# Kernel optimization log

Hardware: AMD Instinct MI355X
Metric: run time of the kernel (lower is better)

## Reference

```python
import jax, jax.numpy as jnp
import numpy as np

EMBED_DIM = 131
SCALE = jnp.sqrt(jnp.float32(131.0))


def setup_inputs() -> dict:
    key = jax.random.key(0)
    ks = jax.random.split(key, 9)
    B, N, D = 8, 2048, EMBED_DIM
    s = 1.0 / np.sqrt(D)  # torch Linear default init scale (uniform bound)
    return {
        "query": jax.random.normal(ks[0], (B, N, D), dtype=jnp.float32),
        "key": jax.random.normal(ks[1], (B, N, D), dtype=jnp.float32),
        "value": jax.random.normal(ks[2], (B, N, D), dtype=jnp.float32),
        "Wq": jax.random.uniform(ks[3], (D, D), jnp.float32, -s, s),
        "bq": jax.random.uniform(ks[4], (D,), jnp.float32, -s, s),
        "Wk": jax.random.uniform(ks[5], (D, D), jnp.float32, -s, s),
        "bk": jax.random.uniform(ks[6], (D,), jnp.float32, -s, s),
        "Wv": jax.random.uniform(ks[7], (D, D), jnp.float32, -s, s),
        "bv": jax.random.uniform(ks[8], (D,), jnp.float32, -s, s),
    }


def reference(query, key, value, Wq, bq, Wk, bk, Wv, bv):
    # Linear projections (torch Linear: x @ W.T + b)
    Q = jnp.einsum("bnd,ed->bne", query, Wq) + bq  # [B, N, D]
    K = jnp.einsum("bnd,ed->bne", key, Wk) + bk    # [B, N, D]
    V = jnp.einsum("bnd,ed->bne", value, Wv) + bv  # [B, N, D]
    # Full attention with hardcoded scale sqrt(131)
    scores = jnp.einsum("bqd,bkd->bqk", Q, K) / SCALE  # [B, N, N]
    weights = jax.nn.softmax(scores, axis=-1)
    return jnp.einsum("bqk,bkd->bqd", weights, V)  # [B, N, D]
```

## Files before the change

kernel.cpp:

```cpp
#include <hip/hip_runtime.h>

#define B_ 8
#define N_ 2048
#define D_ 131
#define COSTR 133
#define SXSTR 164
#define CSTR 168
#define TSTR 72

typedef __attribute__((ext_vector_type(8))) short s16x8;
typedef __attribute__((ext_vector_type(16))) float f32x16;

__device__ __forceinline__ ushort f2bf(float x) {
  uint u = __float_as_uint(x);
  u += 0x7fffu + ((u >> 16) & 1u);
  return (ushort)(u >> 16);
}
__device__ __forceinline__ float bf2f(ushort h) {
  return __uint_as_float(((uint)h) << 16);
}
__device__ __forceinline__ uint bfpair(float a, float b) {
  uint ua = __float_as_uint(a);
  ua += 0x7fffu + ((ua >> 16) & 1u);
  uint ub = __float_as_uint(b);
  ub += 0x7fffu + ((ub >> 16) & 1u);
  return (ua >> 16) | (ub & 0xffff0000u);
}

__device__ __forceinline__ size_t rf32_idx(int nt, int ch, int l) {
  return ((size_t)(nt * 9 + ch) * 64 + l) * 8;
}
__device__ __forceinline__ size_t vf32_idx(int kt, int t2, int dt, int l) {
  return ((size_t)(((kt * 2) + t2) * 5 + dt) * 64 + l) * 8;
}
__device__ __forceinline__ size_t wf32_idx(int p, int h, int et, int ch, int l) {
  return ((size_t)((((p * 2 + h) * 5 + et) * 9) + ch) * 64 + l) * 8;
}

__global__ void cast_w_kernel(const float* __restrict__ Wq,
                              const float* __restrict__ Wk,
                              const float* __restrict__ Wv,
                              ushort* __restrict__ Whl) {
  const int p = blockIdx.x;
  const float* __restrict__ W = (p == 0) ? Wq : (p == 1) ? Wk : Wv;
  for (int i = threadIdx.x; i < 5 * 9 * 64; i += blockDim.x) {
    const int et = i / 576;
    const int rem = i - et * 576;
    const int ch = rem >> 6;
    const int l = rem & 63;
    const int e = et * 32 + (l & 31);
    s16x8 hi, lo;
#pragma unroll
    for (int j = 0; j < 8; ++j) {
      const int d = ch * 16 + (l >> 5) * 8 + j;
      const float val = (e < D_ && d < D_) ? W[e * D_ + d] : 0.f;
      const ushort h = f2bf(val);
      hi[j] = (short)h;
      lo[j] = (short)f2bf(val - bf2f(h));
    }
    *(s16x8*)(Whl + wf32_idx(p, 0, et, ch, l)) = hi;
    *(s16x8*)(Whl + wf32_idx(p, 1, et, ch, l)) = lo;
  }
}

template <int ET0, int NET>
__device__ __forceinline__ void compute_acc(const float* sX,
                                            const ushort* __restrict__ Whl,
                                            int p, int tg, int l,
                                            f32x16 acc[3]) {
  const int l31 = l & 31, hi = l >> 5;
#pragma unroll
  for (int ch = 0; ch < 9; ++ch) {
    const float* xp = sX + (size_t)(32 * tg + l31) * SXSTR + ch * 16 + hi * 8;
    const float4 x0 = *(const float4*)xp;
    const float4 x1 = *(const float4*)(xp + 4);
    const float xv[8] = {x0.x, x0.y, x0.z, x0.w, x1.x, x1.y, x1.z, x1.w};
    s16x8 ah, al;
#pragma unroll
    for (int j = 0; j < 8; ++j) {
      const ushort h = f2bf(xv[j]);
      ah[j] = (short)h;
      al[j] = (short)f2bf(xv[j] - bf2f(h));
    }
    s16x8 bh[NET], bl[NET];
#pragma unroll
    for (int u = 0; u < NET; ++u) {
      bh[u] = *(const s16x8*)(Whl + wf32_idx(p, 0, ET0 + u, ch, l));
      bl[u] = *(const s16x8*)(Whl + wf32_idx(p, 1, ET0 + u, ch, l));
    }
#pragma unroll
    for (int u = 0; u < NET; ++u) {
      acc[u] = __builtin_amdgcn_mfma_f32_32x32x16_bf16(ah, bh[u], acc[u], 0, 0, 0);
      acc[u] = __builtin_amdgcn_mfma_f32_32x32x16_bf16(al, bh[u], acc[u], 0, 0, 0);
      acc[u] = __builtin_amdgcn_mfma_f32_32x32x16_bf16(ah, bl[u], acc[u], 0, 0, 0);
    }
  }
}

template <int ET0, int NET>
__device__ __forceinline__ void epiQK(const f32x16 acc[3], ushort* sC,
                                      const float* sB, int tg, int l,
                                      bool scale) {
  const int l31 = l & 31, hi = l >> 5;
  const float ISC = 0.08737040566610379f;
#pragma unroll
  for (int u = 0; u < NET; ++u) {
    const int e = 32 * (ET0 + u) + l31;
    const float bval = sB[e];
#pragma unroll
    for (int r = 0; r < 16; ++r) {
      const int tok = 32 * tg + (r & 3) + 8 * (r >> 2) + 4 * hi;
      float val = acc[u][r] + bval;
      if (scale) val *= ISC;
      sC[(size_t)tok * CSTR + e] = f2bf(val);
    }
  }
}

template <int ET0, int NET>
__device__ __forceinline__ void epiV(const f32x16 acc[3], ushort* sT,
                                     const float* sB, int tg, int l) {
  const int l31 = l & 31, hi = l >> 5;
#pragma unroll
  for (int u = 0; u < NET; ++u) {
    const int e = 32 * (ET0 + u) + l31;
    if (e < D_) {
      const float bval = sB[e];
#pragma unroll
      for (int g = 0; g < 4; ++g) {
        const float v0 = acc[u][4 * g + 0] + bval;
        const float v1 = acc[u][4 * g + 1] + bval;
        const float v2 = acc[u][4 * g + 2] + bval;
        const float v3 = acc[u][4 * g + 3] + bval;
        uint2 pk;
        pk.x = bfpair(v0, v1);
        pk.y = bfpair(v2, v3);
        *(uint2*)(sT + (size_t)e * TSTR + 32 * tg + 8 * g + 4 * hi) = pk;
      }
    }
  }
}

__global__ __launch_bounds__(256, 3) void proj_gemm(
    const float* __restrict__ q, const float* __restrict__ k,
    const float* __restrict__ v, const float* __restrict__ bq,
    const float* __restrict__ bk, const float* __restrict__ bv,
    const ushort* __restrict__ Whl, ushort* __restrict__ Qf,
    ushort* __restrict__ Kf, ushort* __restrict__ Vf) {
  const int p = blockIdx.y;
  const float* __restrict__ x = (p == 0) ? q : (p == 1) ? k : v;
  const float* __restrict__ bias = (p == 0) ? bq : (p == 1) ? bk : bv;

  __shared__ __align__(16) char smem[64 * SXSTR * 4];
  float* sX = (float*)smem;
  ushort* sC = (ushort*)smem;
  ushort* sT = (ushort*)smem;
  __shared__ float sB[160];

  const int tid = threadIdx.x;
  const int r0 = blockIdx.x * 64;

  {
    const float* __restrict__ xbase = x + (size_t)r0 * D_;
    for (int i = tid; i < 64 * D_ / 4; i += 256) {
      const float4 v4 = *(const float4*)(xbase + i * 4);
      const float vv[4] = {v4.x, v4.y, v4.z, v4.w};
#pragma unroll
      for (int j = 0; j < 4; ++j) {
        const int nl = i * 4 + j;
        const int r = nl / D_;
        const int d = nl - r * D_;
        sX[r * SXSTR + d] = vv[j];
      }
    }
    for (int i = tid; i < 64 * 33; i += 256) {
      const int r = i / 33;
      sX[r * SXSTR + D_ + (i - r * 33)] = 0.f;
    }
  }
  if (tid < 160) sB[tid] = (tid < D_) ? bias[tid] : 0.f;
  __syncthreads();

  const int w = tid >> 6;
  const int l = tid & 63;
  const int tg = w & 1;
  const int eh = w >> 1;

  f32x16 acc[3];
  acc[0] = f32x16{};
  acc[1] = f32x16{};
  acc[2] = f32x16{};
  if (eh == 0)
    compute_acc<0, 3>(sX, Whl, p, tg, l, acc);
  else
    compute_acc<3, 2>(sX, Whl, p, tg, l, acc);

  __syncthreads();

  if (p < 2) {
    if (eh == 0)
      epiQK<0, 3>(acc, sC, sB, tg, l, p == 0);
    else
      epiQK<3, 2>(acc, sC, sB, tg, l, p == 0);
    __syncthreads();
    ushort* __restrict__ dst = (p == 0) ? Qf : Kf;
    const int nt0 = r0 >> 5;
    for (int i = tid; i < 2 * 9 * 64; i += 256) {
      const int ntl = i / 576;
      const int rem = i - ntl * 576;
      const int ch = rem >> 6;
      const int l2 = rem & 63;
      const s16x8 fr = *(const s16x8*)(sC + (size_t)(32 * ntl + (l2 & 31)) * CSTR +
                                       ch * 16 + (l2 >> 5) * 8);
      *(s16x8*)(dst + rf32_idx(nt0 + ntl, ch, l2)) = fr;
    }
  } else {
    for (int i = tid; i < 29 * 64; i += 256) {
      const int e = D_ + (i >> 6);
      sT[(size_t)e * TSTR + (i & 63)] = (e == D_) ? (ushort)0x3F80 : (ushort)0;
    }
    if (eh == 0)
      epiV<0, 3>(acc, sT, sB, tg, l);
    else
      epiV<3, 2>(acc, sT, sB, tg, l);
    __syncthreads();
    const int kt0 = r0 >> 5;
    for (int i = tid; i < 2 * 2 * 5 * 64; i += 256) {
      const int ktl = i / 640;
      const int rem = i - ktl * 640;
      const int t2 = rem / 320;
      const int rem2 = rem - t2 * 320;
      const int dt = rem2 >> 6;
      const int l2 = rem2 & 63;
      const s16x8 fr = *(const s16x8*)(sT + (size_t)(32 * dt + (l2 & 31)) * TSTR +
                                       32 * ktl + 16 * t2 + 8 * (l2 >> 5));
      *(s16x8*)(Vf + vf32_idx(kt0 + ktl, t2, dt, l2)) = fr;
    }
  }
}

__global__ __launch_bounds__(256, 2) void attn_mfma(
    const ushort* __restrict__ Qf, const ushort* __restrict__ Kf,
    const ushort* __restrict__ Vf, float* __restrict__ out) {
  const int id = blockIdx.x;
  const int b = id & 7;
  const int qg = id >> 3;
  const int tid = threadIdx.x;
  const int w = tid >> 6;
  const int l = tid & 63;
  const int l31 = l & 31;
  const int hi = l >> 5;

  __shared__ ushort sQ[9 * 64 * 8];
  __shared__ float cO[4][32][COSTR];
  __shared__ float cm[4][32];

  {
    const uint4* src = (const uint4*)(Qf + rf32_idx(b * 64 + qg, 0, 0));
    uint4* dq = (uint4*)sQ;
    for (int i = tid; i < 576; i += 256) dq[i] = src[i];
  }
  s16x8 kA[9], kB[9];
  const int ktbase = b * 64 + w * 16;
#pragma unroll
  for (int ch = 0; ch < 9; ++ch)
    kA[ch] = *(const s16x8*)(Kf + rf32_idx(ktbase, ch, l));
  __syncthreads();

  f32x16 o[5];
#pragma unroll
  for (int dt = 0; dt < 5; ++dt) o[dt] = f32x16{};
  float mreg = -1e30f;

  auto tile_body = [&](s16x8(&KC)[9], s16x8(&KN)[9], int ktg, int ktgn) {
    s16x8 vf[2][5];
#pragma unroll
    for (int t2 = 0; t2 < 2; ++t2)
#pragma unroll
      for (int dt = 0; dt < 5; ++dt)
        vf[t2][dt] = *(const s16x8*)(Vf + vf32_idx(ktg, t2, dt, l));
#pragma unroll
    for (int ch = 0; ch < 9; ++ch)
      KN[ch] = *(const s16x8*)(Kf + rf32_idx(ktgn, ch, l));
    f32x16 s = f32x16{};
#pragma unroll
    for (int ch = 0; ch < 9; ++ch) {
      const s16x8 qc = *(const s16x8*)(sQ + (ch * 64 + l) * 8);
      s = __builtin_amdgcn_mfma_f32_32x32x16_bf16(KC[ch], qc, s, 0, 0, 0);
    }
    float tm = s[0];
#pragma unroll
    for (int r = 1; r < 16; ++r) tm = fmaxf(tm, s[r]);
    tm = fmaxf(tm, __shfl_xor(tm, 32, 64));
    if (__any(tm > mreg)) {
      const float mo = mreg;
      const float mn = fmaxf(mo, tm);
      mreg = mn;
      const float f = __expf(mo - mn);
      float fr[16];
#pragma unroll
      for (int r = 0; r < 16; ++r)
        fr[r] = __shfl(f, (r & 3) + 8 * (r >> 2) + 4 * hi, 64);
#pragma unroll
      for (int dt = 0; dt < 5; ++dt)
#pragma unroll
        for (int r = 0; r < 16; ++r) o[dt][r] *= fr[r];
    }
    float pp[16];
#pragma unroll
    for (int r = 0; r < 16; ++r) pp[r] = __expf(s[r] - mreg);
    uint pk0[4], pk1[4];
#pragma unroll
    for (int wd = 0; wd < 4; ++wd) {
      pk0[wd] = bfpair(pp[2 * wd], pp[2 * wd + 1]);
      pk1[wd] = bfpair(pp[8 + 2 * wd], pp[8 + 2 * wd + 1]);
    }
    s16x8 pa[2];
    {
      const uint x0 = __shfl_xor(hi ? pk0[0] : pk0[2], 32, 64);
      const uint x1 = __shfl_xor(hi ? pk0[1] : pk0[3], 32, 64);
      uint4 u;
      u.x = hi ? x0 : pk0[0];
      u.y = hi ? x1 : pk0[1];
      u.z = hi ? pk0[2] : x0;
      u.w = hi ? pk0[3] : x1;
      pa[0] = *(s16x8*)&u;
    }
    {
      const uint x0 = __shfl_xor(hi ? pk1[0] : pk1[2], 32, 64);
      const uint x1 = __shfl_xor(hi ? pk1[1] : pk1[3], 32, 64);
      uint4 u;
      u.x = hi ? x0 : pk1[0];
      u.y = hi ? x1 : pk1[1];
      u.z = hi ? pk1[2] : x0;
      u.w = hi ? pk1[3] : x1;
      pa[1] = *(s16x8*)&u;
    }
#pragma unroll
    for (int t2 = 0; t2 < 2; ++t2)
#pragma unroll
      for (int dt = 0; dt < 5; ++dt)
        o[dt] = __builtin_amdgcn_mfma_f32_32x32x16_bf16(pa[t2], vf[t2][dt],
                                                        o[dt], 0, 0, 0);
  };

  for (int i = 0; i < 8; ++i) {
    const int kt = ktbase + 2 * i;
    tile_body(kA, kB, kt, kt + 1);
    tile_body(kB, kA, kt + 1, (i < 7) ? kt + 2 : kt + 1);
  }

  if (l < 32) cm[w][l] = mreg;
#pragma unroll
  for (int dt = 0; dt < 5; ++dt) {
    const int d = 32 * dt + l31;
    if (d <= D_) {
#pragma unroll
      for (int r = 0; r < 16; ++r) {
        const int row = (r & 3) + 8 * (r >> 2) + 4 * hi;
        cO[w][row][d] = o[dt][r];
      }
    }
  }
  __syncthreads();
  for (int rr = 0; rr < 8; ++rr) {
    const int row = w * 8 + rr;
    const float m0 = cm[0][row], m1 = cm[1][row];
    const float m2 = cm[2][row], m3 = cm[3][row];
    const float M = fmaxf(fmaxf(m0, m1), fmaxf(m2, m3));
    const float e0 = __expf(m0 - M);
    const float e1 = __expf(m1 - M);
    const float e2 = __expf(m2 - M);
    const float e3 = __expf(m3 - M);
    const float lsum = cO[0][row][D_] * e0 + cO[1][row][D_] * e1 +
                       cO[2][row][D_] * e2 + cO[3][row][D_] * e3;
    const float inv = 1.f / lsum;
    float* orow = out + ((size_t)b * N_ + qg * 32 + row) * D_;
    for (int d = l; d < D_; d += 64) {
      const float val = cO[0][row][d] * e0 + cO[1][row][d] * e1 +
                        cO[2][row][d] * e2 + cO[3][row][d] * e3;
      orow[d] = val * inv;
    }
  }
}

extern "C" void kernel_launch(void* const* d_in, const int* in_sizes, int n_in,
                              void* d_out, int out_size, void* d_ws,
                              size_t ws_size, hipStream_t stream) {
  const float* q = (const float*)d_in[0];
  const float* k = (const float*)d_in[1];
  const float* v = (const float*)d_in[2];
  const float* Wq = (const float*)d_in[3];
  const float* bq = (const float*)d_in[4];
  const float* Wk = (const float*)d_in[5];
  const float* bk = (const float*)d_in[6];
  const float* Wv = (const float*)d_in[7];
  const float* bv = (const float*)d_in[8];
  float* out = (float*)d_out;

  char* wsb = (char*)d_ws;
  ushort* Qf = (ushort*)(wsb);
  ushort* Kf = (ushort*)(wsb + 4718592);
  ushort* Vf = (ushort*)(wsb + 9437184);
  ushort* Whl = (ushort*)(wsb + 14680064);

  hipLaunchKernelGGL(cast_w_kernel, dim3(3), dim3(256), 0, stream, Wq, Wk, Wv,
                     Whl);
  hipLaunchKernelGGL(proj_gemm, dim3(256, 3), dim3(256), 0, stream, q, k, v,
                     bq, bk, bv, Whl, Qf, Kf, Vf);
  hipLaunchKernelGGL(attn_mfma, dim3(512), dim3(256), 0, stream, Qf, Kf, Vf,
                     out);
}
```

Measured before the change: 68.93 us.

## Process two query tiles per block to reuse K/V fragments

Each attention block now handles 64 query rows (two 32-row tiles) instead of 32, sharing each loaded K and V fragment across both tiles. The grid shrinks from 512 to 256 blocks. The launch bound drops to one block per SM because doubled accumulators raise register pressure. This halves global K/V traffic per query row, but lowers occupancy and leaves fewer blocks than there are CUs on MI355X (256), which risks poor load balance and less latency hiding.

```diff
diff --git a/kernel.cpp b/kernel.cpp
--- a/kernel.cpp
+++ b/kernel.cpp
@@ -239,26 +239,26 @@
   }
 }
 
-__global__ __launch_bounds__(256, 2) void attn_mfma(
+__global__ __launch_bounds__(256, 1) void attn_mfma(
     const ushort* __restrict__ Qf, const ushort* __restrict__ Kf,
     const ushort* __restrict__ Vf, float* __restrict__ out) {
   const int id = blockIdx.x;
   const int b = id & 7;
-  const int qg = id >> 3;
+  const int qg2 = id >> 3;
   const int tid = threadIdx.x;
   const int w = tid >> 6;
   const int l = tid & 63;
   const int l31 = l & 31;
   const int hi = l >> 5;
 
-  __shared__ ushort sQ[9 * 64 * 8];
+  __shared__ ushort sQ[2 * 9 * 64 * 8];
   __shared__ float cO[4][32][COSTR];
   __shared__ float cm[4][32];
 
   {
-    const uint4* src = (const uint4*)(Qf + rf32_idx(b * 64 + qg, 0, 0));
+    const uint4* src = (const uint4*)(Qf + rf32_idx(b * 64 + qg2 * 2, 0, 0));
     uint4* dq = (uint4*)sQ;
-    for (int i = tid; i < 576; i += 256) dq[i] = src[i];
+    for (int i = tid; i < 1152; i += 256) dq[i] = src[i];
   }
   s16x8 kA[9], kB[9];
   const int ktbase = b * 64 + w * 16;
@@ -267,10 +267,13 @@
     kA[ch] = *(const s16x8*)(Kf + rf32_idx(ktbase, ch, l));
   __syncthreads();
 
-  f32x16 o[5];
-#pragma unroll
-  for (int dt = 0; dt < 5; ++dt) o[dt] = f32x16{};
-  float mreg = -1e30f;
+  f32x16 o0[5], o1[5];
+#pragma unroll
+  for (int dt = 0; dt < 5; ++dt) {
+    o0[dt] = f32x16{};
+    o1[dt] = f32x16{};
+  }
+  float mreg0 = -1e30f, mreg1 = -1e30f;
 
   auto tile_body = [&](s16x8(&KC)[9], s16x8(&KN)[9], int ktg, int ktgn) {
     s16x8 vf[2][5];
@@ -282,66 +285,72 @@
 #pragma unroll
     for (int ch = 0; ch < 9; ++ch)
       KN[ch] = *(const s16x8*)(Kf + rf32_idx(ktgn, ch, l));
-    f32x16 s = f32x16{};
+    f32x16 s0 = f32x16{}, s1 = f32x16{};
 #pragma unroll
     for (int ch = 0; ch < 9; ++ch) {
-      const s16x8 qc = *(const s16x8*)(sQ + (ch * 64 + l) * 8);
-      s = __builtin_amdgcn_mfma_f32_32x32x16_bf16(KC[ch], qc, s, 0, 0, 0);
-    }
-    float tm = s[0];
-#pragma unroll
-    for (int r = 1; r < 16; ++r) tm = fmaxf(tm, s[r]);
-    tm = fmaxf(tm, __shfl_xor(tm, 32, 64));
-    if (__any(tm > mreg)) {
-      const float mo = mreg;
-      const float mn = fmaxf(mo, tm);
-      mreg = mn;
-      const float f = __expf(mo - mn);
-      float fr[16];
-#pragma unroll
-      for (int r = 0; r < 16; ++r)
-        fr[r] = __shfl(f, (r & 3) + 8 * (r >> 2) + 4 * hi, 64);
-#pragma unroll
-      for (int dt = 0; dt < 5; ++dt)
-#pragma unroll
-        for (int r = 0; r < 16; ++r) o[dt][r] *= fr[r];
-    }
-    float pp[16];
-#pragma unroll
-    for (int r = 0; r < 16; ++r) pp[r] = __expf(s[r] - mreg);
-    uint pk0[4], pk1[4];
-#pragma unroll
-    for (int wd = 0; wd < 4; ++wd) {
-      pk0[wd] = bfpair(pp[2 * wd], pp[2 * wd + 1]);
-      pk1[wd] = bfpair(pp[8 + 2 * wd], pp[8 + 2 * wd + 1]);
-    }
-    s16x8 pa[2];
-    {
-      const uint x0 = __shfl_xor(hi ? pk0[0] : pk0[2], 32, 64);
-      const uint x1 = __shfl_xor(hi ? pk0[1] : pk0[3], 32, 64);
-      uint4 u;
-      u.x = hi ? x0 : pk0[0];
-      u.y = hi ? x1 : pk0[1];
-      u.z = hi ? pk0[2] : x0;
-      u.w = hi ? pk0[3] : x1;
-      pa[0] = *(s16x8*)&u;
-    }
-    {
-      const uint x0 = __shfl_xor(hi ? pk1[0] : pk1[2], 32, 64);
-      const uint x1 = __shfl_xor(hi ? pk1[1] : pk1[3], 32, 64);
-      uint4 u;
-      u.x = hi ? x0 : pk1[0];
-      u.y = hi ? x1 : pk1[1];
-      u.z = hi ? pk1[2] : x0;
-      u.w = hi ? pk1[3] : x1;
-      pa[1] = *(s16x8*)&u;
-    }
-#pragma unroll
-    for (int t2 = 0; t2 < 2; ++t2)
-#pragma unroll
-      for (int dt = 0; dt < 5; ++dt)
-        o[dt] = __builtin_amdgcn_mfma_f32_32x32x16_bf16(pa[t2], vf[t2][dt],
-                                                        o[dt], 0, 0, 0);
+      const s16x8 qc0 = *(const s16x8*)(sQ + (ch * 64 + l) * 8);
+      const s16x8 qc1 = *(const s16x8*)(sQ + ((9 + ch) * 64 + l) * 8);
+      s0 = __builtin_amdgcn_mfma_f32_32x32x16_bf16(KC[ch], qc0, s0, 0, 0, 0);
+      s1 = __builtin_amdgcn_mfma_f32_32x32x16_bf16(KC[ch], qc1, s1, 0, 0, 0);
+    }
+    auto softmax_pv = [&](f32x16& s, float& mreg, f32x16(&og)[5]) {
+      float tm = s[0];
+#pragma unroll
+      for (int r = 1; r < 16; ++r) tm = fmaxf(tm, s[r]);
+      tm = fmaxf(tm, __shfl_xor(tm, 32, 64));
+      if (__any(tm > mreg)) {
+        const float mo = mreg;
+        const float mn = fmaxf(mo, tm);
+        mreg = mn;
+        const float f = __expf(mo - mn);
+        float fr[16];
+#pragma unroll
+        for (int r = 0; r < 16; ++r)
+          fr[r] = __shfl(f, (r & 3) + 8 * (r >> 2) + 4 * hi, 64);
+#pragma unroll
+        for (int dt = 0; dt < 5; ++dt)
+#pragma unroll
+          for (int r = 0; r < 16; ++r) og[dt][r] *= fr[r];
+      }
+      float pp[16];
+#pragma unroll
+      for (int r = 0; r < 16; ++r) pp[r] = __expf(s[r] - mreg);
+      uint pk0[4], pk1[4];
+#pragma unroll
+      for (int wd = 0; wd < 4; ++wd) {
+        pk0[wd] = bfpair(pp[2 * wd], pp[2 * wd + 1]);
+        pk1[wd] = bfpair(pp[8 + 2 * wd], pp[8 + 2 * wd + 1]);
+      }
+      s16x8 pa[2];
+      {
+        const uint x0 = __shfl_xor(hi ? pk0[0] : pk0[2], 32, 64);
+        const uint x1 = __shfl_xor(hi ? pk0[1] : pk0[3], 32, 64);
+        uint4 u;
+        u.x = hi ? x0 : pk0[0];
+        u.y = hi ? x1 : pk0[1];
+        u.z = hi ? pk0[2] : x0;
+        u.w = hi ? pk0[3] : x1;
+        pa[0] = *(s16x8*)&u;
+      }
+      {
+        const uint x0 = __shfl_xor(hi ? pk1[0] : pk1[2], 32, 64);
+        const uint x1 = __shfl_xor(hi ? pk1[1] : pk1[3], 32, 64);
+        uint4 u;
+        u.x = hi ? x0 : pk1[0];
+        u.y = hi ? x1 : pk1[1];
+        u.z = hi ? pk1[2] : x0;
+        u.w = hi ? pk1[3] : x1;
+        pa[1] = *(s16x8*)&u;
+      }
+#pragma unroll
+      for (int t2 = 0; t2 < 2; ++t2)
+#pragma unroll
+        for (int dt = 0; dt < 5; ++dt)
+          og[dt] = __builtin_amdgcn_mfma_f32_32x32x16_bf16(pa[t2], vf[t2][dt],
+                                                           og[dt], 0, 0, 0);
+    };
+    softmax_pv(s0, mreg0, o0);
+    softmax_pv(s1, mreg1, o1);
   };
 
   for (int i = 0; i < 8; ++i) {
@@ -350,36 +359,40 @@
     tile_body(kB, kA, kt + 1, (i < 7) ? kt + 2 : kt + 1);
   }
 
-  if (l < 32) cm[w][l] = mreg;
-#pragma unroll
-  for (int dt = 0; dt < 5; ++dt) {
-    const int d = 32 * dt + l31;
-    if (d <= D_) {
-#pragma unroll
-      for (int r = 0; r < 16; ++r) {
-        const int row = (r & 3) + 8 * (r >> 2) + 4 * hi;
-        cO[w][row][d] = o[dt][r];
-      }
-    }
-  }
-  __syncthreads();
-  for (int rr = 0; rr < 8; ++rr) {
-    const int row = w * 8 + rr;
-    const float m0 = cm[0][row], m1 = cm[1][row];
-    const float m2 = cm[2][row], m3 = cm[3][row];
-    const float M = fmaxf(fmaxf(m0, m1), fmaxf(m2, m3));
-    const float e0 = __expf(m0 - M);
-    const float e1 = __expf(m1 - M);
-    const float e2 = __expf(m2 - M);
-    const float e3 = __expf(m3 - M);
-    const float lsum = cO[0][row][D_] * e0 + cO[1][row][D_] * e1 +
-                       cO[2][row][D_] * e2 + cO[3][row][D_] * e3;
-    const float inv = 1.f / lsum;
-    float* orow = out + ((size_t)b * N_ + qg * 32 + row) * D_;
-    for (int d = l; d < D_; d += 64) {
-      const float val = cO[0][row][d] * e0 + cO[1][row][d] * e1 +
-                        cO[2][row][d] * e2 + cO[3][row][d] * e3;
-      orow[d] = val * inv;
+#pragma unroll
+  for (int c = 0; c < 2; ++c) {
+    if (c) __syncthreads();
+    if (l < 32) cm[w][l] = c ? mreg1 : mreg0;
+#pragma unroll
+    for (int dt = 0; dt < 5; ++dt) {
+      const int d = 32 * dt + l31;
+      if (d <= D_) {
+#pragma unroll
+        for (int r = 0; r < 16; ++r) {
+          const int row = (r & 3) + 8 * (r >> 2) + 4 * hi;
+          cO[w][row][d] = c ? o1[dt][r] : o0[dt][r];
+        }
+      }
+    }
+    __syncthreads();
+    for (int rr = 0; rr < 8; ++rr) {
+      const int row = w * 8 + rr;
+      const float m0 = cm[0][row], m1 = cm[1][row];
+      const float m2 = cm[2][row], m3 = cm[3][row];
+      const float M = fmaxf(fmaxf(m0, m1), fmaxf(m2, m3));
+      const float e0 = __expf(m0 - M);
+      const float e1 = __expf(m1 - M);
+      const float e2 = __expf(m2 - M);
+      const float e3 = __expf(m3 - M);
+      const float lsum = cO[0][row][D_] * e0 + cO[1][row][D_] * e1 +
+                         cO[2][row][D_] * e2 + cO[3][row][D_] * e3;
+      const float inv = 1.f / lsum;
+      float* orow = out + ((size_t)b * N_ + qg2 * 64 + c * 32 + row) * D_;
+      for (int d = l; d < D_; d += 64) {
+        const float val = cO[0][row][d] * e0 + cO[1][row][d] * e1 +
+                          cO[2][row][d] * e2 + cO[3][row][d] * e3;
+        orow[d] = val * inv;
+      }
     }
   }
 }
@@ -408,6 +421,6 @@
                      Whl);
   hipLaunchKernelGGL(proj_gemm, dim3(256, 3), dim3(256), 0, stream, q, k, v,
                      bq, bk, bv, Whl, Qf, Kf, Vf);
-  hipLaunchKernelGGL(attn_mfma, dim3(512), dim3(256), 0, stream, Qf, Kf, Vf,
+  hipLaunchKernelGGL(attn_mfma, dim3(256), dim3(256), 0, stream, Qf, Kf, Vf,
                      out);
 }
```

Result: slower. 114.0 us (+65.4%).

## Software-pipeline QK^T MFMA of next tile with softmax and PV of current

Applied to the files above, without the earlier changes.

Restructures the attention inner loop so the QK^T MFMA for the next key tile is issued before the softmax and PV MFMAs of the current tile. Two score accumulators and a two-deep K register prefetch let matrix and vector/exp work interleave. The row max also becomes a tree reduction and the loop is fully unrolled. The cost is more VGPR pressure from the extra score and K registers, which could lower occupancy or cause spills.

```diff
diff --git a/kernel.cpp b/kernel.cpp
--- a/kernel.cpp
+++ b/kernel.cpp
@@ -260,11 +260,14 @@
     uint4* dq = (uint4*)sQ;
     for (int i = tid; i < 576; i += 256) dq[i] = src[i];
   }
+  const int ktbase = b * 64 + w * 16;
   s16x8 kA[9], kB[9];
-  const int ktbase = b * 64 + w * 16;
 #pragma unroll
   for (int ch = 0; ch < 9; ++ch)
     kA[ch] = *(const s16x8*)(Kf + rf32_idx(ktbase, ch, l));
+#pragma unroll
+  for (int ch = 0; ch < 9; ++ch)
+    kB[ch] = *(const s16x8*)(Kf + rf32_idx(ktbase + 1, ch, l));
   __syncthreads();
 
   f32x16 o[5];
@@ -272,25 +275,24 @@
   for (int dt = 0; dt < 5; ++dt) o[dt] = f32x16{};
   float mreg = -1e30f;
 
-  auto tile_body = [&](s16x8(&KC)[9], s16x8(&KN)[9], int ktg, int ktgn) {
-    s16x8 vf[2][5];
-#pragma unroll
-    for (int t2 = 0; t2 < 2; ++t2)
-#pragma unroll
-      for (int dt = 0; dt < 5; ++dt)
-        vf[t2][dt] = *(const s16x8*)(Vf + vf32_idx(ktg, t2, dt, l));
-#pragma unroll
-    for (int ch = 0; ch < 9; ++ch)
-      KN[ch] = *(const s16x8*)(Kf + rf32_idx(ktgn, ch, l));
-    f32x16 s = f32x16{};
-#pragma unroll
-    for (int ch = 0; ch < 9; ++ch) {
-      const s16x8 qc = *(const s16x8*)(sQ + (ch * 64 + l) * 8);
-      s = __builtin_amdgcn_mfma_f32_32x32x16_bf16(KC[ch], qc, s, 0, 0, 0);
-    }
-    float tm = s[0];
-#pragma unroll
-    for (int r = 1; r < 16; ++r) tm = fmaxf(tm, s[r]);
+  f32x16 sA = f32x16{};
+#pragma unroll
+  for (int ch = 0; ch < 9; ++ch) {
+    const s16x8 qc = *(const s16x8*)(sQ + (ch * 64 + l) * 8);
+    sA = __builtin_amdgcn_mfma_f32_32x32x16_bf16(kA[ch], qc, sA, 0, 0, 0);
+  }
+  f32x16 sB;
+
+  auto softmax_pv = [&](f32x16& s, const s16x8(&vf)[2][5]) {
+    float t0 = fmaxf(s[0], s[1]), t1 = fmaxf(s[2], s[3]);
+    float t2_ = fmaxf(s[4], s[5]), t3 = fmaxf(s[6], s[7]);
+    float t4 = fmaxf(s[8], s[9]), t5 = fmaxf(s[10], s[11]);
+    float t6 = fmaxf(s[12], s[13]), t7 = fmaxf(s[14], s[15]);
+    t0 = fmaxf(t0, t1);
+    t2_ = fmaxf(t2_, t3);
+    t4 = fmaxf(t4, t5);
+    t6 = fmaxf(t6, t7);
+    float tm = fmaxf(fmaxf(t0, t2_), fmaxf(t4, t6));
     tm = fmaxf(tm, __shfl_xor(tm, 32, 64));
     if (__any(tm > mreg)) {
       const float mo = mreg;
@@ -344,10 +346,50 @@
                                                         o[dt], 0, 0, 0);
   };
 
+#pragma unroll
   for (int i = 0; i < 8; ++i) {
-    const int kt = ktbase + 2 * i;
-    tile_body(kA, kB, kt, kt + 1);
-    tile_body(kB, kA, kt + 1, (i < 7) ? kt + 2 : kt + 1);
+    {
+      s16x8 vf[2][5];
+#pragma unroll
+      for (int t2 = 0; t2 < 2; ++t2)
+#pragma unroll
+        for (int dt = 0; dt < 5; ++dt)
+          vf[t2][dt] =
+              *(const s16x8*)(Vf + vf32_idx(ktbase + 2 * i, t2, dt, l));
+      const int tp = (2 * i + 2 < 16) ? (2 * i + 2) : 15;
+#pragma unroll
+      for (int ch = 0; ch < 9; ++ch)
+        kA[ch] = *(const s16x8*)(Kf + rf32_idx(ktbase + tp, ch, l));
+      sB = f32x16{};
+#pragma unroll
+      for (int ch = 0; ch < 9; ++ch) {
+        const s16x8 qc = *(const s16x8*)(sQ + (ch * 64 + l) * 8);
+        sB = __builtin_amdgcn_mfma_f32_32x32x16_bf16(kB[ch], qc, sB, 0, 0, 0);
+      }
+      softmax_pv(sA, vf);
+    }
+    {
+      s16x8 vf[2][5];
+#pragma unroll
+      for (int t2 = 0; t2 < 2; ++t2)
+#pragma unroll
+        for (int dt = 0; dt < 5; ++dt)
+          vf[t2][dt] =
+              *(const s16x8*)(Vf + vf32_idx(ktbase + 2 * i + 1, t2, dt, l));
+      const int tp = (2 * i + 3 < 16) ? (2 * i + 3) : 15;
+#pragma unroll
+      for (int ch = 0; ch < 9; ++ch)
+        kB[ch] = *(const s16x8*)(Kf + rf32_idx(ktbase + tp, ch, l));
+      if (i < 7) {
+        sA = f32x16{};
+#pragma unroll
+        for (int ch = 0; ch < 9; ++ch) {
+          const s16x8 qc = *(const s16x8*)(sQ + (ch * 64 + l) * 8);
+          sA = __builtin_amdgcn_mfma_f32_32x32x16_bf16(kA[ch], qc, sA, 0, 0, 0);
+        }
+      }
+      softmax_pv(sB, vf);
+    }
   }
 
   if (l < 32) cm[w][l] = mreg;
```

Measured after the change: 68.49 us (median of 2 runs). About the same (-0.6%).

## Process two key tiles per iteration with exp2 softmax and prefetched K/V

Applied to the files above, without the earlier changes.

Restructures the attention loop so each iteration computes two 32-key score tiles together and does one joint max and rescale for both. K fragments for the next pair and V fragments for the next tile are loaded ahead of use, and the loop is fully unrolled. The 1/sqrt(D) scale folded into Q now includes log2(e), so every exponential becomes a native exp2. The intent is fewer rescale checks, more independent MFMAs in flight and better hiding of load latency, at the cost of higher register pressure under the 2-block launch bound.

```diff
diff --git a/kernel.cpp b/kernel.cpp
--- a/kernel.cpp
+++ b/kernel.cpp
@@ -26,6 +26,10 @@
   ub += 0x7fffu + ((ub >> 16) & 1u);
   return (ua >> 16) | (ub & 0xffff0000u);
 }
+__device__ __forceinline__ float f3(float a, float b, float c) {
+  return fmaxf(fmaxf(a, b), c);
+}
+__device__ __forceinline__ float ex2(float x) { return __builtin_exp2f(x); }
 
 __device__ __forceinline__ size_t rf32_idx(int nt, int ch, int l) {
   return ((size_t)(nt * 9 + ch) * 64 + l) * 8;
@@ -102,7 +106,7 @@
                                       const float* sB, int tg, int l,
                                       bool scale) {
   const int l31 = l & 31, hi = l >> 5;
-  const float ISC = 0.08737040566610379f;
+  const float ISC = 0.1260488539f;
 #pragma unroll
   for (int u = 0; u < NET; ++u) {
     const int e = 32 * (ET0 + u) + l31;
@@ -255,16 +259,27 @@
   __shared__ float cO[4][32][COSTR];
   __shared__ float cm[4][32];
 
+  const int ktbase = b * 64 + w * 16;
+
+  s16x8 kA[9], kB[9];
+#pragma unroll
+  for (int ch = 0; ch < 9; ++ch)
+    kA[ch] = *(const s16x8*)(Kf + rf32_idx(ktbase, ch, l));
+#pragma unroll
+  for (int ch = 0; ch < 9; ++ch)
+    kB[ch] = *(const s16x8*)(Kf + rf32_idx(ktbase + 1, ch, l));
+  s16x8 va[2][5];
+#pragma unroll
+  for (int t2 = 0; t2 < 2; ++t2)
+#pragma unroll
+    for (int dt = 0; dt < 5; ++dt)
+      va[t2][dt] = *(const s16x8*)(Vf + vf32_idx(ktbase, t2, dt, l));
+
   {
     const uint4* src = (const uint4*)(Qf + rf32_idx(b * 64 + qg, 0, 0));
     uint4* dq = (uint4*)sQ;
     for (int i = tid; i < 576; i += 256) dq[i] = src[i];
   }
-  s16x8 kA[9], kB[9];
-  const int ktbase = b * 64 + w * 16;
-#pragma unroll
-  for (int ch = 0; ch < 9; ++ch)
-    kA[ch] = *(const s16x8*)(Kf + rf32_idx(ktbase, ch, l));
   __syncthreads();
 
   f32x16 o[5];
@@ -272,82 +287,109 @@
   for (int dt = 0; dt < 5; ++dt) o[dt] = f32x16{};
   float mreg = -1e30f;
 
-  auto tile_body = [&](s16x8(&KC)[9], s16x8(&KN)[9], int ktg, int ktgn) {
-    s16x8 vf[2][5];
-#pragma unroll
-    for (int t2 = 0; t2 < 2; ++t2)
-#pragma unroll
-      for (int dt = 0; dt < 5; ++dt)
-        vf[t2][dt] = *(const s16x8*)(Vf + vf32_idx(ktg, t2, dt, l));
-#pragma unroll
-    for (int ch = 0; ch < 9; ++ch)
-      KN[ch] = *(const s16x8*)(Kf + rf32_idx(ktgn, ch, l));
-    f32x16 s = f32x16{};
+  auto xchg = [&](const uint pk[4]) -> s16x8 {
+    const uint x0 = __shfl_xor(hi ? pk[0] : pk[2], 32, 64);
+    const uint x1 = __shfl_xor(hi ? pk[1] : pk[3], 32, 64);
+    uint4 u;
+    u.x = hi ? x0 : pk[0];
+    u.y = hi ? x1 : pk[1];
+    u.z = hi ? pk[2] : x0;
+    u.w = hi ? pk[3] : x1;
+    return *(s16x8*)&u;
+  };
+
+#pragma unroll
+  for (int i = 0; i < 8; ++i) {
+    const int t0 = ktbase + 2 * i;
+    f32x16 sA = f32x16{}, sB = f32x16{};
 #pragma unroll
     for (int ch = 0; ch < 9; ++ch) {
       const s16x8 qc = *(const s16x8*)(sQ + (ch * 64 + l) * 8);
-      s = __builtin_amdgcn_mfma_f32_32x32x16_bf16(KC[ch], qc, s, 0, 0, 0);
-    }
-    float tm = s[0];
-#pragma unroll
-    for (int r = 1; r < 16; ++r) tm = fmaxf(tm, s[r]);
-    tm = fmaxf(tm, __shfl_xor(tm, 32, 64));
-    if (__any(tm > mreg)) {
-      const float mo = mreg;
-      const float mn = fmaxf(mo, tm);
-      mreg = mn;
-      const float f = __expf(mo - mn);
-      float fr[16];
-#pragma unroll
-      for (int r = 0; r < 16; ++r)
-        fr[r] = __shfl(f, (r & 3) + 8 * (r >> 2) + 4 * hi, 64);
+      sA = __builtin_amdgcn_mfma_f32_32x32x16_bf16(kA[ch], qc, sA, 0, 0, 0);
+      sB = __builtin_amdgcn_mfma_f32_32x32x16_bf16(kB[ch], qc, sB, 0, 0, 0);
+    }
+    if (i < 7) {
+#pragma unroll
+      for (int ch = 0; ch < 9; ++ch)
+        kA[ch] = *(const s16x8*)(Kf + rf32_idx(t0 + 2, ch, l));
+#pragma unroll
+      for (int ch = 0; ch < 9; ++ch)
+        kB[ch] = *(const s16x8*)(Kf + rf32_idx(t0 + 3, ch, l));
+    }
+    {
+      const float m0 = f3(sA[0], sA[1], sA[2]);
+      const float m1 = f3(sA[3], sA[4], sA[5]);
+      const float m2 = f3(sA[6], sA[7], sA[8]);
+      const float m3 = f3(sA[9], sA[10], sA[11]);
+      const float m4 = f3(sA[12], sA[13], sA[14]);
+      const float m5 = f3(sA[15], sB[0], sB[1]);
+      const float m6 = f3(sB[2], sB[3], sB[4]);
+      const float m7 = f3(sB[5], sB[6], sB[7]);
+      const float m8 = f3(sB[8], sB[9], sB[10]);
+      const float m9 = f3(sB[11], sB[12], sB[13]);
+      const float ma = fmaxf(sB[14], sB[15]);
+      float tm = f3(f3(m0, m1, m2), f3(m3, m4, m5), f3(m6, m7, m8));
+      tm = f3(tm, m9, ma);
+      tm = fmaxf(tm, __shfl_xor(tm, 32, 64));
+      if (__any(tm > mreg)) {
+        const float mo = mreg;
+        const float mn = fmaxf(mo, tm);
+        mreg = mn;
+        const float f = ex2(mo - mn);
+        float fr[16];
+#pragma unroll
+        for (int r = 0; r < 16; ++r)
+          fr[r] = __shfl(f, (r & 3) + 8 * (r >> 2) + 4 * hi, 64);
+#pragma unroll
+        for (int dt = 0; dt < 5; ++dt)
+#pragma unroll
+          for (int r = 0; r < 16; ++r) o[dt][r] *= fr[r];
+      }
+    }
+    s16x8 paA[2], paB[2];
+    {
+      uint pk0[4], pk1[4];
+#pragma unroll
+      for (int wd = 0; wd < 4; ++wd) {
+        pk0[wd] = bfpair(ex2(sA[2 * wd] - mreg), ex2(sA[2 * wd + 1] - mreg));
+        pk1[wd] =
+            bfpair(ex2(sA[8 + 2 * wd] - mreg), ex2(sA[8 + 2 * wd + 1] - mreg));
+      }
+      paA[0] = xchg(pk0);
+      paA[1] = xchg(pk1);
+#pragma unroll
+      for (int wd = 0; wd < 4; ++wd) {
+        pk0[wd] = bfpair(ex2(sB[2 * wd] - mreg), ex2(sB[2 * wd + 1] - mreg));
+        pk1[wd] =
+            bfpair(ex2(sB[8 + 2 * wd] - mreg), ex2(sB[8 + 2 * wd + 1] - mreg));
+      }
+      paB[0] = xchg(pk0);
+      paB[1] = xchg(pk1);
+    }
+#pragma unroll
+    for (int t2 = 0; t2 < 2; ++t2)
 #pragma unroll
       for (int dt = 0; dt < 5; ++dt)
-#pragma unroll
-        for (int r = 0; r < 16; ++r) o[dt][r] *= fr[r];
-    }
-    float pp[16];
-#pragma unroll
-    for (int r = 0; r < 16; ++r) pp[r] = __expf(s[r] - mreg);
-    uint pk0[4], pk1[4];
-#pragma unroll
-    for (int wd = 0; wd < 4; ++wd) {
-      pk0[wd] = bfpair(pp[2 * wd], pp[2 * wd + 1]);
-      pk1[wd] = bfpair(pp[8 + 2 * wd], pp[8 + 2 * wd + 1]);
-    }
-    s16x8 pa[2];
-    {
-      const uint x0 = __shfl_xor(hi ? pk0[0] : pk0[2], 32, 64);
-      const uint x1 = __shfl_xor(hi ? pk0[1] : pk0[3], 32, 64);
-      uint4 u;
-      u.x = hi ? x0 : pk0[0];
-      u.y = hi ? x1 : pk0[1];
-      u.z = hi ? pk0[2] : x0;
-      u.w = hi ? pk0[3] : x1;
-      pa[0] = *(s16x8*)&u;
-    }
-    {
-      const uint x0 = __shfl_xor(hi ? pk1[0] : pk1[2], 32, 64);
-      const uint x1 = __shfl_xor(hi ? pk1[1] : pk1[3], 32, 64);
-      uint4 u;
-      u.x = hi ? x0 : pk1[0];
-      u.y = hi ? x1 : pk1[1];
-      u.z = hi ? pk1[2] : x0;
-      u.w = hi ? pk1[3] : x1;
-      pa[1] = *(s16x8*)&u;
-    }
+        o[dt] = __builtin_amdgcn_mfma_f32_32x32x16_bf16(paA[t2], va[t2][dt],
+                                                        o[dt], 0, 0, 0);
 #pragma unroll
     for (int t2 = 0; t2 < 2; ++t2)
 #pragma unroll
       for (int dt = 0; dt < 5; ++dt)
-        o[dt] = __builtin_amdgcn_mfma_f32_32x32x16_bf16(pa[t2], vf[t2][dt],
+        va[t2][dt] = *(const s16x8*)(Vf + vf32_idx(t0 + 1, t2, dt, l));
+#pragma unroll
+    for (int t2 = 0; t2 < 2; ++t2)
+#pragma unroll
+      for (int dt = 0; dt < 5; ++dt)
+        o[dt] = __builtin_amdgcn_mfma_f32_32x32x16_bf16(paB[t2], va[t2][dt],
                                                         o[dt], 0, 0, 0);
-  };
-
-  for (int i = 0; i < 8; ++i) {
-    const int kt = ktbase + 2 * i;
-    tile_body(kA, kB, kt, kt + 1);
-    tile_body(kB, kA, kt + 1, (i < 7) ? kt + 2 : kt + 1);
+    if (i < 7) {
+#pragma unroll
+      for (int t2 = 0; t2 < 2; ++t2)
+#pragma unroll
+        for (int dt = 0; dt < 5; ++dt)
+          va[t2][dt] = *(const s16x8*)(Vf + vf32_idx(t0 + 2, t2, dt, l));
+    }
   }
 
   if (l < 32) cm[w][l] = mreg;
@@ -368,10 +410,10 @@
     const float m0 = cm[0][row], m1 = cm[1][row];
     const float m2 = cm[2][row], m3 = cm[3][row];
     const float M = fmaxf(fmaxf(m0, m1), fmaxf(m2, m3));
-    const float e0 = __expf(m0 - M);
-    const float e1 = __expf(m1 - M);
-    const float e2 = __expf(m2 - M);
-    const float e3 = __expf(m3 - M);
+    const float e0 = ex2(m0 - M);
+    const float e1 = ex2(m1 - M);
+    const float e2 = ex2(m2 - M);
+    const float e3 = ex2(m3 - M);
     const float lsum = cO[0][row][D_] * e0 + cO[1][row][D_] * e1 +
                        cO[2][row][D_] * e2 + cO[3][row][D_] * e3;
     const float inv = 1.f / lsum;
```

Result: no change. 70.07 us (+1.7%).
